# Kernel optimization log

Hardware: AMD Instinct MI355X
Metric: run time of the kernel (lower is better)

The kernel has to match this reference:

```python
import jax, jax.numpy as jnp
import numpy as np

DELTA_VAR = 0.1
DELTA_DIST = 0.3
ALPHA = 1.0
BETA = 1.0
C = 2048  # number of superpixels (static; torch derives it as sp_seg.max()+1)


def setup_inputs() -> dict:
    key = jax.random.key(0)
    k1, k2, k3, k4 = jax.random.split(key, 4)
    B, E, H, W = 4, 32, 512, 512
    n_edges = 8192
    embeddings = jax.random.normal(k1, (B, E, H, W), dtype=jnp.float32)
    sp_seg = jax.random.randint(k2, (B, 1, H, W), 0, C)
    edges = jax.random.randint(k3, (B, 2, n_edges), 0, C)
    weights = jax.random.uniform(k4, (B, n_edges), dtype=jnp.float32)
    return {"embeddings": embeddings, "sp_seg": sp_seg, "edges": edges, "weights": weights}


def _per_sample(emb, seg, edg, w):
    # emb: [E,H,W], seg: [1,H,W], edg: [2,n_edges], w: [n_edges]
    E = emb.shape[0]
    N = emb.shape[1] * emb.shape[2]
    emb_f = emb.reshape(E, N).T              # [N,E]
    seg_f = seg.reshape(N)                   # [N]
    counts = jax.ops.segment_sum(jnp.ones((N,), emb.dtype), seg_f, num_segments=C)  # [C]
    sums = jax.ops.segment_sum(emb_f, seg_f, num_segments=C)                         # [C,E]
    means = sums / jnp.maximum(counts, 1.0)[:, None]
    norm = jnp.sqrt(jnp.sum(means * means, axis=-1, keepdims=True))
    means = means / jnp.maximum(norm, 1e-10)  # L2-normalized superpixel means [C,E]
    # intra-superpixel distance: 1 - <mean_sp(pix), emb(pix)> per pixel
    d = 1.0 - jnp.sum(means[seg_f] * emb_f, axis=-1)  # [N]
    intra = jnp.sum(jnp.maximum(d - DELTA_VAR, 0.0) / counts[seg_f]) / C
    # inter-superpixel distance along RAG edges
    f0 = means[edg[0]]                       # [n_edges,E]
    f1 = means[edg[1]]
    inter = 1.0 - jnp.sum(f0 * f1, axis=-1)  # [n_edges]
    inter = jnp.maximum(DELTA_DIST - inter * w, 0.0)
    inter = jnp.sum(inter) / edg.shape[1]
    return ALPHA * inter + BETA * intra


def reference(embeddings, sp_seg, edges, weights):
    per_sample = jax.vmap(_per_sample)(embeddings, sp_seg, edges, weights)  # [B]
    return jnp.sum(per_sample)  # scalar (torch sums over batch then .mean() of a 1-elem tensor)
```

## Files before the change

kernel.cpp:

```cpp
#include <hip/hip_runtime.h>

#define BN 4
#define EN 32
#define NPIX (512 * 512)
#define CSEG 2048
#define NEDGE 8192

#define DELTA_VAR 0.1f
#define DELTA_DIST 0.3f

#define FP_SCALE 256.0f
#define FP_INV (1.0 / 256.0)
#define FP_BIAS 16.0f
#define NGRP 11
#define MASK21 ((1ull << 21) - 1)

typedef unsigned long long u64;


__global__ __launch_bounds__(512) void rag_accum(
    const float* __restrict__ emb, const int* __restrict__ seg,
    u64* __restrict__ sums64) {
  __shared__ u64 lsum[2 * CSEG];

  const int blk = blockIdx.x;
  const int pb = blk & 31;
  const int t = blk >> 5;
  const int fam = t % 6;
  const int b = t / 6;

  const int nz = (fam < 5) ? 2 * CSEG : CSEG;
  for (int i = threadIdx.x; i < nz; i += 512) lsum[i] = 0ull;
  __syncthreads();

  const int ppb = NPIX / 32;
  const int p0 = pb * ppb;
  const int* __restrict__ sb = seg + (size_t)b * NPIX;

  if (fam < 5) {
    const float* __restrict__ eb = emb + ((size_t)b * EN + 6 * fam) * NPIX;
    for (int p = p0 + threadIdx.x; p < p0 + ppb; p += 512) {
      const int s = sb[p];
      u64 pk0, pk1;
      {
        const unsigned int q0 =
            (unsigned int)__float2int_rn((eb[p] + FP_BIAS) * FP_SCALE);
        const unsigned int q1 =
            (unsigned int)__float2int_rn((eb[p + NPIX] + FP_BIAS) * FP_SCALE);
        const unsigned int q2 =
            (unsigned int)__float2int_rn((eb[p + 2 * NPIX] + FP_BIAS) * FP_SCALE);
        pk0 = (u64)q0 | ((u64)q1 << 21) | ((u64)q2 << 42);
      }
      {
        const unsigned int q3 =
            (unsigned int)__float2int_rn((eb[p + 3 * NPIX] + FP_BIAS) * FP_SCALE);
        const unsigned int q4 =
            (unsigned int)__float2int_rn((eb[p + 4 * NPIX] + FP_BIAS) * FP_SCALE);
        const unsigned int q5 =
            (unsigned int)__float2int_rn((eb[p + 5 * NPIX] + FP_BIAS) * FP_SCALE);
        pk1 = (u64)q3 | ((u64)q4 << 21) | ((u64)q5 << 42);
      }
      atomicAdd(&lsum[s], pk0);
      atomicAdd(&lsum[CSEG + s], pk1);
    }
    __syncthreads();
    const int g0 = 2 * fam;
    for (int i = threadIdx.x; i < 2 * CSEG; i += 512) {
      const int g = g0 + (i >> 11);
      const int c = i & (CSEG - 1);
      atomicAdd(&sums64[((size_t)g * BN + b) * CSEG + c], lsum[i]);
    }
  } else {
    const float* __restrict__ eb = emb + ((size_t)b * EN + 30) * NPIX;
    for (int p = p0 + threadIdx.x; p < p0 + ppb; p += 512) {
      const int s = sb[p];
      const unsigned int q0 =
          (unsigned int)__float2int_rn((eb[p] + FP_BIAS) * FP_SCALE);
      const unsigned int q1 =
          (unsigned int)__float2int_rn((eb[p + NPIX] + FP_BIAS) * FP_SCALE);
      atomicAdd(&lsum[s], (u64)q0 | ((u64)q1 << 21) | (1ull << 42));
    }
    __syncthreads();
    for (int i = threadIdx.x; i < CSEG; i += 512) {
      atomicAdd(&sums64[((size_t)10 * BN + b) * CSEG + i], lsum[i]);
    }
  }
}

__global__ __launch_bounds__(256) void rag_finalize(
    const u64* __restrict__ sums64, float* __restrict__ invcnt,
    float* __restrict__ means) {
  const int idx = blockIdx.x * 256 + threadIdx.x;
  if (idx >= BN * CSEG) return;
  const int b = idx >> 11;
  const int c = idx & (CSEG - 1);
  const u64 sq10 = sums64[((size_t)10 * BN + b) * CSEG + c];
  const int cnt = (int)(sq10 >> 42);
  const double bias = (double)FP_BIAS * (double)cnt;
  const double inv = 1.0 / (double)(cnt > 1 ? cnt : 1);
  float m[EN];
  double nrm = 0.0;
#pragma unroll
  for (int g = 0; g < 10; g++) {
    const u64 sq = sums64[((size_t)g * BN + b) * CSEG + c];
    const double s0 = (double)(sq & MASK21) * FP_INV - bias;
    const double s1 = (double)((sq >> 21) & MASK21) * FP_INV - bias;
    const double s2 = (double)(sq >> 42) * FP_INV - bias;
    const double m0 = s0 * inv, m1 = s1 * inv, m2 = s2 * inv;
    m[3 * g] = (float)m0;
    m[3 * g + 1] = (float)m1;
    m[3 * g + 2] = (float)m2;
    nrm += m0 * m0 + m1 * m1 + m2 * m2;
  }
  {
    const double s0 = (double)(sq10 & MASK21) * FP_INV - bias;
    const double s1 = (double)((sq10 >> 21) & MASK21) * FP_INV - bias;
    const double m0 = s0 * inv, m1 = s1 * inv;
    m[30] = (float)m0;
    m[31] = (float)m1;
    nrm += m0 * m0 + m1 * m1;
  }
  const float sc = (float)(1.0 / fmax(sqrt(nrm), 1e-10));
  invcnt[idx] = (float)inv;
  float* __restrict__ mb = means + (size_t)idx * EN;
#pragma unroll
  for (int e = 0; e < EN; e++) mb[e] = m[e] * sc;
}

__global__ __launch_bounds__(256) void rag_intra(
    const float* __restrict__ emb, const int* __restrict__ seg,
    const float* __restrict__ invcnt, const float* __restrict__ means,
    float* __restrict__ out) {
  const int t = blockIdx.x * 256 + threadIdx.x;
  const int b = t >> 16;
  const int p4 = (t & 65535) << 2;
  const int4 s4 = *(const int4*)(seg + (size_t)b * NPIX + p4);
  const float* __restrict__ eb = emb + (size_t)b * EN * NPIX + p4;
  const float* __restrict__ mb = means + (size_t)b * CSEG * EN;
  const float* __restrict__ m0 = mb + (size_t)s4.x * EN;
  const float* __restrict__ m1 = mb + (size_t)s4.y * EN;
  const float* __restrict__ m2 = mb + (size_t)s4.z * EN;
  const float* __restrict__ m3 = mb + (size_t)s4.w * EN;
  float d0 = 0.f, d1 = 0.f, d2 = 0.f, d3 = 0.f;
#pragma unroll
  for (int e = 0; e < EN; e++) {
    const float4 v = *(const float4*)(eb + (size_t)e * NPIX);
    d0 += m0[e] * v.x;
    d1 += m1[e] * v.y;
    d2 += m2[e] * v.z;
    d3 += m3[e] * v.w;
  }
  const float* __restrict__ ic = invcnt + b * CSEG;
  float acc = 0.f;
  {
    const float u0 = 1.0f - d0 - DELTA_VAR;
    const float u1 = 1.0f - d1 - DELTA_VAR;
    const float u2 = 1.0f - d2 - DELTA_VAR;
    const float u3 = 1.0f - d3 - DELTA_VAR;
    if (u0 > 0.f) acc += u0 * ic[s4.x];
    if (u1 > 0.f) acc += u1 * ic[s4.y];
    if (u2 > 0.f) acc += u2 * ic[s4.z];
    if (u3 > 0.f) acc += u3 * ic[s4.w];
  }
  for (int o = 32; o > 0; o >>= 1) acc += __shfl_down(acc, o, 64);
  __shared__ float wsum[4];
  const int lane = threadIdx.x & 63;
  const int wid = threadIdx.x >> 6;
  if (lane == 0) wsum[wid] = acc;
  __syncthreads();
  if (threadIdx.x == 0) {
    atomicAdd(out, (wsum[0] + wsum[1] + wsum[2] + wsum[3]) * (1.0f / CSEG));
  }
}

#define JTHREADS 256
__global__ __launch_bounds__(JTHREADS) void rag_inter(
    const int* __restrict__ edges, const float* __restrict__ weights,
    const float* __restrict__ means, float* __restrict__ out) {
  const int idx = blockIdx.x * JTHREADS + threadIdx.x;
  float val = 0.0f;
  if (idx < BN * NEDGE) {
    const int b = idx >> 13;
    const int k = idx & (NEDGE - 1);
    const int e0 = edges[(size_t)b * 2 * NEDGE + k];
    const int e1 = edges[(size_t)b * 2 * NEDGE + NEDGE + k];
    const float w = weights[idx];
    const float4* __restrict__ ma =
        (const float4*)(means + ((size_t)b * CSEG + e0) * EN);
    const float4* __restrict__ mc =
        (const float4*)(means + ((size_t)b * CSEG + e1) * EN);
    float dot = 0.0f;
#pragma unroll
    for (int e4 = 0; e4 < EN / 4; e4++) {
      const float4 a = ma[e4];
      const float4 c = mc[e4];
      dot += a.x * c.x + a.y * c.y + a.z * c.z + a.w * c.w;
    }
    val = fmaxf(DELTA_DIST - (1.0f - dot) * w, 0.0f);
  }
  for (int o = 32; o > 0; o >>= 1) val += __shfl_down(val, o, 64);
  __shared__ float wsum[JTHREADS / 64];
  const int lane = threadIdx.x & 63;
  const int wid = threadIdx.x >> 6;
  if (lane == 0) wsum[wid] = val;
  __syncthreads();
  if (threadIdx.x == 0) {
    float bsum = 0.0f;
#pragma unroll
    for (int w = 0; w < JTHREADS / 64; w++) bsum += wsum[w];
    atomicAdd(out, bsum * (1.0f / NEDGE));
  }
}

extern "C" void kernel_launch(void* const* d_in, const int* in_sizes, int n_in,
                              void* d_out, int out_size, void* d_ws, size_t ws_size,
                              hipStream_t stream) {
  const float* emb = (const float*)d_in[0];
  const int* seg = (const int*)d_in[1];
  const int* edges = (const int*)d_in[2];
  const float* weights = (const float*)d_in[3];
  float* out = (float*)d_out;

  u64* sums64 = (u64*)d_ws;
  float* invcnt = (float*)(sums64 + (size_t)NGRP * BN * CSEG);
  float* means = invcnt + (size_t)BN * CSEG;

  hipMemsetAsync(d_out, 0, (size_t)out_size * sizeof(float), stream);
  hipMemsetAsync(d_ws, 0, (size_t)NGRP * BN * CSEG * 8, stream);

  rag_accum<<<32 * 6 * BN, 512, 0, stream>>>(emb, seg, sums64);
  rag_finalize<<<(BN * CSEG + 255) / 256, 256, 0, stream>>>(sums64, invcnt, means);
  rag_intra<<<BN * NPIX / 4 / 256, 256, 0, stream>>>(emb, seg, invcnt, means, out);
  rag_inter<<<(BN * NEDGE + JTHREADS - 1) / JTHREADS, JTHREADS, 0, stream>>>(
      edges, weights, means, out);
}
```

Baseline: 87.93 us.

## Repack segment sums as four 16-bit lanes in shared memory with separate count pass

The accumulation kernel now packs four quantized embedding channels into 16-bit fields of a single shared u64 per superpixel, halving shared memory per block, and widens them to 32-bit lanes only when flushing to global memory. Pixel counts move to a dedicated block family that uses 32-bit shared atomics. The grid doubles the pixel splits (64 per sample), giving more, smaller blocks with less per-block shared memory, which should raise occupancy. The quantization scale drops to 128, which coarsens precision, and 16-bit per-block fields could overflow if a block puts many pixels into one superpixel.

```diff
diff --git a/kernel.cpp b/kernel.cpp
--- a/kernel.cpp
+++ b/kernel.cpp
@@ -9,115 +9,93 @@
 #define DELTA_VAR 0.1f
 #define DELTA_DIST 0.3f
 
-#define FP_SCALE 256.0f
-#define FP_INV (1.0 / 256.0)
+#define FP_SCALE 128.0f
+#define FP_INV (1.0 / 128.0)
 #define FP_BIAS 16.0f
-#define NGRP 11
-#define MASK21 ((1ull << 21) - 1)
 
 typedef unsigned long long u64;
 
 
 __global__ __launch_bounds__(512) void rag_accum(
     const float* __restrict__ emb, const int* __restrict__ seg,
-    u64* __restrict__ sums64) {
-  __shared__ u64 lsum[2 * CSEG];
+    u64* __restrict__ gsum, unsigned int* __restrict__ gcount) {
+  __shared__ u64 lsum[CSEG];
 
   const int blk = blockIdx.x;
-  const int pb = blk & 31;
-  const int t = blk >> 5;
-  const int fam = t % 6;
-  const int b = t / 6;
-
-  const int nz = (fam < 5) ? 2 * CSEG : CSEG;
-  for (int i = threadIdx.x; i < nz; i += 512) lsum[i] = 0ull;
-  __syncthreads();
-
-  const int ppb = NPIX / 32;
+  const int pb = blk & 63;
+  const int t = blk >> 6;
+  const int fam = t % 9;
+  const int b = t / 9;
+
+  const int ppb = NPIX / 64;
   const int p0 = pb * ppb;
   const int* __restrict__ sb = seg + (size_t)b * NPIX;
 
-  if (fam < 5) {
-    const float* __restrict__ eb = emb + ((size_t)b * EN + 6 * fam) * NPIX;
-    for (int p = p0 + threadIdx.x; p < p0 + ppb; p += 512) {
-      const int s = sb[p];
-      u64 pk0, pk1;
-      {
-        const unsigned int q0 =
-            (unsigned int)__float2int_rn((eb[p] + FP_BIAS) * FP_SCALE);
-        const unsigned int q1 =
-            (unsigned int)__float2int_rn((eb[p + NPIX] + FP_BIAS) * FP_SCALE);
-        const unsigned int q2 =
-            (unsigned int)__float2int_rn((eb[p + 2 * NPIX] + FP_BIAS) * FP_SCALE);
-        pk0 = (u64)q0 | ((u64)q1 << 21) | ((u64)q2 << 42);
-      }
-      {
-        const unsigned int q3 =
-            (unsigned int)__float2int_rn((eb[p + 3 * NPIX] + FP_BIAS) * FP_SCALE);
-        const unsigned int q4 =
-            (unsigned int)__float2int_rn((eb[p + 4 * NPIX] + FP_BIAS) * FP_SCALE);
-        const unsigned int q5 =
-            (unsigned int)__float2int_rn((eb[p + 5 * NPIX] + FP_BIAS) * FP_SCALE);
-        pk1 = (u64)q3 | ((u64)q4 << 21) | ((u64)q5 << 42);
-      }
-      atomicAdd(&lsum[s], pk0);
-      atomicAdd(&lsum[CSEG + s], pk1);
-    }
-    __syncthreads();
-    const int g0 = 2 * fam;
-    for (int i = threadIdx.x; i < 2 * CSEG; i += 512) {
-      const int g = g0 + (i >> 11);
-      const int c = i & (CSEG - 1);
-      atomicAdd(&sums64[((size_t)g * BN + b) * CSEG + c], lsum[i]);
-    }
-  } else {
-    const float* __restrict__ eb = emb + ((size_t)b * EN + 30) * NPIX;
+  if (fam < 8) {
+    for (int i = threadIdx.x; i < CSEG; i += 512) lsum[i] = 0ull;
+    __syncthreads();
+    const float* __restrict__ eb = emb + ((size_t)b * EN + 4 * fam) * NPIX;
     for (int p = p0 + threadIdx.x; p < p0 + ppb; p += 512) {
       const int s = sb[p];
       const unsigned int q0 =
           (unsigned int)__float2int_rn((eb[p] + FP_BIAS) * FP_SCALE);
       const unsigned int q1 =
           (unsigned int)__float2int_rn((eb[p + NPIX] + FP_BIAS) * FP_SCALE);
-      atomicAdd(&lsum[s], (u64)q0 | ((u64)q1 << 21) | (1ull << 42));
-    }
-    __syncthreads();
+      const unsigned int q2 =
+          (unsigned int)__float2int_rn((eb[p + 2 * NPIX] + FP_BIAS) * FP_SCALE);
+      const unsigned int q3 =
+          (unsigned int)__float2int_rn((eb[p + 3 * NPIX] + FP_BIAS) * FP_SCALE);
+      const u64 pk = (u64)q0 | ((u64)q1 << 16) | ((u64)q2 << 32) | ((u64)q3 << 48);
+      atomicAdd(&lsum[s], pk);
+    }
+    __syncthreads();
+    u64* __restrict__ g0 = gsum + ((size_t)(2 * fam) * BN + b) * CSEG;
+    u64* __restrict__ g1 = gsum + ((size_t)(2 * fam + 1) * BN + b) * CSEG;
     for (int i = threadIdx.x; i < CSEG; i += 512) {
-      atomicAdd(&sums64[((size_t)10 * BN + b) * CSEG + i], lsum[i]);
+      const u64 v = lsum[i];
+      if (v) {
+        const u64 lo2 = (v & 0xffffull) | ((v & 0xffff0000ull) << 16);
+        const u64 hi2 = ((v >> 32) & 0xffffull) | ((v >> 48) << 32);
+        atomicAdd(&g0[i], lo2);
+        atomicAdd(&g1[i], hi2);
+      }
+    }
+  } else {
+    unsigned int* __restrict__ lcnt = (unsigned int*)lsum;
+    for (int i = threadIdx.x; i < CSEG; i += 512) lcnt[i] = 0u;
+    __syncthreads();
+    for (int p = p0 + threadIdx.x; p < p0 + ppb; p += 512) {
+      atomicAdd(&lcnt[sb[p]], 1u);
+    }
+    __syncthreads();
+    unsigned int* __restrict__ gc = gcount + (size_t)b * CSEG;
+    for (int i = threadIdx.x; i < CSEG; i += 512) {
+      const unsigned int v = lcnt[i];
+      if (v) atomicAdd(&gc[i], v);
     }
   }
 }
 
 __global__ __launch_bounds__(256) void rag_finalize(
-    const u64* __restrict__ sums64, float* __restrict__ invcnt,
-    float* __restrict__ means) {
+    const u64* __restrict__ gsum, const unsigned int* __restrict__ gcount,
+    float* __restrict__ invcnt, float* __restrict__ means) {
   const int idx = blockIdx.x * 256 + threadIdx.x;
   if (idx >= BN * CSEG) return;
   const int b = idx >> 11;
   const int c = idx & (CSEG - 1);
-  const u64 sq10 = sums64[((size_t)10 * BN + b) * CSEG + c];
-  const int cnt = (int)(sq10 >> 42);
+  const int cnt = (int)gcount[idx];
   const double bias = (double)FP_BIAS * (double)cnt;
   const double inv = 1.0 / (double)(cnt > 1 ? cnt : 1);
   float m[EN];
   double nrm = 0.0;
 #pragma unroll
-  for (int g = 0; g < 10; g++) {
-    const u64 sq = sums64[((size_t)g * BN + b) * CSEG + c];
-    const double s0 = (double)(sq & MASK21) * FP_INV - bias;
-    const double s1 = (double)((sq >> 21) & MASK21) * FP_INV - bias;
-    const double s2 = (double)(sq >> 42) * FP_INV - bias;
-    const double m0 = s0 * inv, m1 = s1 * inv, m2 = s2 * inv;
-    m[3 * g] = (float)m0;
-    m[3 * g + 1] = (float)m1;
-    m[3 * g + 2] = (float)m2;
-    nrm += m0 * m0 + m1 * m1 + m2 * m2;
-  }
-  {
-    const double s0 = (double)(sq10 & MASK21) * FP_INV - bias;
-    const double s1 = (double)((sq10 >> 21) & MASK21) * FP_INV - bias;
+  for (int k = 0; k < 16; k++) {
+    const u64 v = gsum[((size_t)k * BN + b) * CSEG + c];
+    const double s0 = (double)(unsigned int)(v & 0xffffffffull) * FP_INV - bias;
+    const double s1 = (double)(unsigned int)(v >> 32) * FP_INV - bias;
     const double m0 = s0 * inv, m1 = s1 * inv;
-    m[30] = (float)m0;
-    m[31] = (float)m1;
+    m[2 * k] = (float)m0;
+    m[2 * k + 1] = (float)m1;
     nrm += m0 * m0 + m1 * m1;
   }
   const float sc = (float)(1.0 / fmax(sqrt(nrm), 1e-10));
@@ -221,15 +199,18 @@
   const float* weights = (const float*)d_in[3];
   float* out = (float*)d_out;
 
-  u64* sums64 = (u64*)d_ws;
-  float* invcnt = (float*)(sums64 + (size_t)NGRP * BN * CSEG);
+  u64* gsum = (u64*)d_ws;
+  unsigned int* gcount = (unsigned int*)(gsum + (size_t)16 * BN * CSEG);
+  float* invcnt = (float*)(gcount + (size_t)BN * CSEG);
   float* means = invcnt + (size_t)BN * CSEG;
 
   hipMemsetAsync(d_out, 0, (size_t)out_size * sizeof(float), stream);
-  hipMemsetAsync(d_ws, 0, (size_t)NGRP * BN * CSEG * 8, stream);
-
-  rag_accum<<<32 * 6 * BN, 512, 0, stream>>>(emb, seg, sums64);
-  rag_finalize<<<(BN * CSEG + 255) / 256, 256, 0, stream>>>(sums64, invcnt, means);
+  hipMemsetAsync(d_ws, 0,
+                 (size_t)16 * BN * CSEG * 8 + (size_t)BN * CSEG * 4, stream);
+
+  rag_accum<<<64 * 9 * BN, 512, 0, stream>>>(emb, seg, gsum, gcount);
+  rag_finalize<<<(BN * CSEG + 255) / 256, 256, 0, stream>>>(gsum, gcount,
+                                                            invcnt, means);
   rag_intra<<<BN * NPIX / 4 / 256, 256, 0, stream>>>(emb, seg, invcnt, means, out);
   rag_inter<<<(BN * NEDGE + JTHREADS - 1) / JTHREADS, JTHREADS, 0, stream>>>(
       edges, weights, means, out);
```

Result: slower. 118.4 us (+34.7%).
